# Performance work log

Hardware: AMD Instinct MI355X
Metric: run time of the kernel (lower is better)

The kernel has to match this reference:

```python
import jax, jax.numpy as jnp
import numpy as np

N, E, T, NORB, H, C = 10000, 100000, 200000, 9, 128, 64


def _normalize(v, eps=1e-12):
    # F.normalize: v / max(||v||_2, eps) along last dim
    n = jnp.linalg.norm(v, axis=-1, keepdims=True)
    return v / jnp.maximum(n, eps)


def setup_inputs() -> dict:
    key = jax.random.key(0)
    ks = jax.random.split(key, 24)
    p = lambda i, shape, scale=0.05: jax.random.normal(ks[i], shape, jnp.float32) * scale
    return {
        "x": jax.random.normal(ks[0], (N, H), jnp.float32),
        "cji": jax.random.normal(ks[1], (E, NORB, C), jnp.float32),
        "cutoff_w": jax.random.uniform(ks[2], (E,), jnp.float32),
        "rb": jax.random.normal(ks[3], (E, NORB), jnp.float32),
        "shb": jax.random.normal(ks[4], (T, NORB), jnp.float32),
        "idx_i": jax.random.randint(ks[5], (E,), 0, N),
        "idx_j": jax.random.randint(ks[6], (E,), 0, N),
        "tri_idx_k": jax.random.randint(ks[7], (T,), 0, N),
        "edge_idx_kj": jax.random.randint(ks[8], (T,), 0, E),
        "edge_idx_ji": jax.random.randint(ks[9], (T,), 0, E),
        "w_node": p(10, (H, 2 * C)),
        "b_node": jnp.zeros((2 * C,), jnp.float32),
        "w_c1": p(11, (C, C)),  # coeffs_dim == C here
        "w_c2": p(12, (C, C)),
        "w_t1": p(13, (C, C)),
        "b_t1": jnp.zeros((C,), jnp.float32),
        "w_t2": p(14, (C, C)),
        "b_t2": jnp.zeros((C,), jnp.float32),
        "w_basis": p(15, (C, C)),
        "w_n1": p(16, (2 * C, C)),
        "b_n1": jnp.zeros((C,), jnp.float32),
        "w_n2": p(17, (C, C)),
        "b_n2": jnp.zeros((C,), jnp.float32),
        "w_out": p(18, (C, H)),
    }


def reference(x, cji, cutoff_w, rb, shb, idx_i, idx_j, tri_idx_k, edge_idx_kj,
              edge_idx_ji, w_node, b_node, w_c1, w_c2, w_t1, b_t1, w_t2, b_t2,
              w_basis, w_n1, b_n1, w_n2, b_n2, w_out):
    silu = jax.nn.silu
    x_before = x
    # node_weight -> chunk into (x, xk), each (N, C)
    h = x @ w_node + b_node
    x1, xk = h[:, :C], h[:, C:]
    # f_coeffs: two bias-free Dense + SiLU, per (E, n_orb) position
    cji = silu(silu(cji @ w_c1) @ w_c2)  # (E, NORB, C)
    # cutoff weighting on radial basis
    rb = rb * cutoff_w[:, None]  # (E, NORB)
    # triplet gather + contraction over orbital axis d
    ckj = cji[edge_idx_kj]  # (T, NORB, C)
    three_body_orbs = jnp.einsum("td,tdh->th", rb[edge_idx_kj] * shb, ckj)  # (T, C)
    three_body_orbs = _normalize(three_body_orbs)
    xk_g = jax.nn.sigmoid(xk[tri_idx_k])  # (T, C)
    three_body_w = three_body_orbs * xk_g
    # scatter-sum triplets -> edges, then f_three MLP
    agg = jax.ops.segment_sum(three_body_w, edge_idx_ji, num_segments=E)  # (E, C)
    three_body_w = silu(silu(agg @ w_t1 + b_t1) @ w_t2 + b_t2)  # (E, C)
    cji = cji + cji * three_body_w[:, None, :]  # (E, NORB, C)
    # LCAO weights: contract radial basis with coefficients
    lcao_w = jnp.einsum("ed,edh->eh", rb, cji)  # (E, C)
    lcao_w = _normalize(lcao_w) @ w_basis
    # f_node on gathered endpoint features
    pair = jnp.concatenate([x1[idx_i], x1[idx_j]], axis=-1)  # (E, 2C)
    fnode = silu(silu(pair @ w_n1 + b_n1) @ w_n2 + b_n2)  # (E, C)
    msg = lcao_w * fnode
    out = x_before + jax.ops.segment_sum(msg, idx_i, num_segments=N) @ w_out
    return out
```

## Files before the change

### kernel.cpp

```cpp
#include <hip/hip_runtime.h>
#include <math.h>

typedef __attribute__((ext_vector_type(8))) short bf16x8;
typedef __attribute__((ext_vector_type(4))) float f32x4;
typedef __attribute__((ext_vector_type(4))) unsigned int uint32x4;
typedef unsigned int uint32;
typedef unsigned short ushort;

#define N_NODES 10000
#define E_EDGES 100000
#define T_TRI   200000
#define NORB    9
#define H_DIM   128
#define C_DIM   64
#define LSTR    68

__device__ __forceinline__ ushort f2b_rtne(float f) {
  uint32 u = __float_as_uint(f);
  u += 0x7FFFu + ((u >> 16) & 1u);
  return (ushort)(u >> 16);
}
__device__ __forceinline__ uint32 rtne2(float a, float b) {
  uint32 ua = __float_as_uint(a), ub = __float_as_uint(b);
  ua += 0x7FFFu + ((ua >> 16) & 1u);
  ub += 0x7FFFu + ((ub >> 16) & 1u);
  return (ua >> 16) | (ub & 0xFFFF0000u);
}
__device__ __forceinline__ uint32 trunc2(float a, float b) {
  return (__float_as_uint(a) >> 16) | (__float_as_uint(b) & 0xFFFF0000u);
}
__device__ __forceinline__ float b2f(ushort u) {
  return __uint_as_float(((uint32)u) << 16);
}
__device__ __forceinline__ float silu_f(float x) {
  return x * __builtin_amdgcn_rcpf(1.0f + __expf(-x));
}
__device__ __forceinline__ float sigmoid_f(float x) {
  return __builtin_amdgcn_rcpf(1.0f + __expf(-x));
}
__device__ __forceinline__ float rl(float v, int k) {
  return __uint_as_float(__builtin_amdgcn_readlane(__float_as_uint(v), k));
}
__device__ __forceinline__ f32x4 mfma16(bf16x8 a, bf16x8 b, f32x4 c) {
  return __builtin_amdgcn_mfma_f32_16x16x32_bf16(a, b, c, 0, 0, 0);
}
#define LDS_FENCE() asm volatile("s_waitcnt lgkmcnt(0)" ::: "memory")

__device__ __forceinline__ bf16x8 pack8(const float* p) {
  f32x4 v0 = *(const f32x4*)p;
  f32x4 v1 = *(const f32x4*)(p + 4);
  uint32x4 u;
  u[0] = trunc2(v0[0], v0[1]);
  u[1] = trunc2(v0[2], v0[3]);
  u[2] = trunc2(v1[0], v1[1]);
  u[3] = trunc2(v1[2], v1[3]);
  return __builtin_bit_cast(bf16x8, u);
}
__device__ __forceinline__ bf16x8 bfrag_w(const float* W, int kt, int ct, int lane) {
  const float* p = W + (size_t)(kt * 32 + ((lane >> 4) * 8)) * 64 + ct * 16 + (lane & 15);
  bf16x8 r;
#pragma unroll
  for (int b = 0; b < 8; ++b) r[b] = (short)f2b_rtne(p[(size_t)b * 64]);
  return r;
}

__global__ __launch_bounds__(128) void k_node_mlp(
    const float* __restrict__ x, const float* __restrict__ w_node,
    const float* __restrict__ b_node, ushort* __restrict__ x1b,
    ushort* __restrict__ sigxkb) {
  __shared__ float xs[H_DIM];
  int n = blockIdx.x;
  int c = threadIdx.x;
  xs[c] = x[(size_t)n * H_DIM + c];
  __syncthreads();
  float acc = b_node[c];
#pragma unroll 8
  for (int k = 0; k < H_DIM; ++k)
    acc = fmaf(xs[k], w_node[k * H_DIM + c], acc);
  if (c < C_DIM)
    x1b[(size_t)n * C_DIM + c] = f2b_rtne(acc);
  else
    sigxkb[(size_t)n * C_DIM + (c - C_DIM)] = f2b_rtne(sigmoid_f(acc));
}

__global__ __launch_bounds__(256) void k_cji_mlp_mfma(
    const float* __restrict__ cji, const float* __restrict__ w_c1,
    const float* __restrict__ w_c2, ushort* __restrict__ cji2) {
  __shared__ __align__(16) float lds_all[4][16 * LSTR];
  int lane = threadIdx.x & 63;
  float* lds = lds_all[threadIdx.x >> 6];
  int wid = (blockIdx.x * 256 + (int)threadIdx.x) >> 6;
  int nw = (gridDim.x * 256) >> 6;
  bf16x8 w1f[2][4], w2f[2][4];
#pragma unroll
  for (int kt = 0; kt < 2; ++kt)
#pragma unroll
    for (int ct = 0; ct < 4; ++ct) {
      w1f[kt][ct] = bfrag_w(w_c1, kt, ct, lane);
      w2f[kt][ct] = bfrag_w(w_c2, kt, ct, lane);
    }
  const int nstrips = (E_EDGES * NORB) / 16;
  int l15 = lane & 15, g = lane >> 4;
  int wrow = g * 4, wcol = l15;
  f32x4 z = {0.f, 0.f, 0.f, 0.f};
  for (int s = wid; s < nstrips; s += nw) {
    const float* ap = cji + (size_t)(s * 16 + l15) * 64 + g * 8;
    bf16x8 a0 = pack8(ap), a1 = pack8(ap + 32);
#pragma unroll
    for (int ct = 0; ct < 4; ++ct) {
      f32x4 acc = mfma16(a0, w1f[0][ct], z);
      acc = mfma16(a1, w1f[1][ct], acc);
#pragma unroll
      for (int r = 0; r < 4; ++r)
        lds[(wrow + r) * LSTR + ct * 16 + wcol] = silu_f(acc[r]);
    }
    LDS_FENCE();
    bf16x8 t0 = pack8(lds + l15 * LSTR + g * 8);
    bf16x8 t1 = pack8(lds + l15 * LSTR + 32 + g * 8);
#pragma unroll
    for (int ct = 0; ct < 4; ++ct) {
      f32x4 acc = mfma16(t0, w2f[0][ct], z);
      acc = mfma16(t1, w2f[1][ct], acc);
#pragma unroll
      for (int r = 0; r < 4; ++r)
        lds[(wrow + r) * LSTR + ct * 16 + wcol] = silu_f(acc[r]);
    }
    LDS_FENCE();
    const float* lp = lds + l15 * LSTR + g * 16;
    f32x4 v0 = *(const f32x4*)lp;
    f32x4 v1 = *(const f32x4*)(lp + 4);
    f32x4 v2 = *(const f32x4*)(lp + 8);
    f32x4 v3 = *(const f32x4*)(lp + 12);
    uint32x4 o0, o1;
    o0[0] = rtne2(v0[0], v0[1]); o0[1] = rtne2(v0[2], v0[3]);
    o0[2] = rtne2(v1[0], v1[1]); o0[3] = rtne2(v1[2], v1[3]);
    o1[0] = rtne2(v2[0], v2[1]); o1[1] = rtne2(v2[2], v2[3]);
    o1[2] = rtne2(v3[0], v3[1]); o1[3] = rtne2(v3[2], v3[3]);
    uint32x4* dst = (uint32x4*)(cji2 + (size_t)(s * 16 + l15) * 64 + g * 16);
    dst[0] = o0;
    dst[1] = o1;
  }
}

__global__ __launch_bounds__(256) void k_triplet(
    const ushort* __restrict__ cji2, const float* __restrict__ rb,
    const float* __restrict__ cutoff_w, const float* __restrict__ shb,
    const int* __restrict__ tri_idx_k, const int* __restrict__ edge_idx_kj,
    const int* __restrict__ edge_idx_ji, const ushort* __restrict__ sigxkb,
    float* __restrict__ agg) {
  int lane = threadIdx.x & 63;
  int wid = (blockIdx.x * 256 + (int)threadIdx.x) >> 6;
  int nw = (gridDim.x * 256) >> 6;
  for (int t = wid; t < T_TRI; t += nw) {
    int e = edge_idx_kj[t];
    float cw = cutoff_w[e];
    const ushort* crow = cji2 + (size_t)e * (NORB * C_DIM);
    float acc = 0.f;
#pragma unroll
    for (int d = 0; d < NORB; ++d) {
      float coeff = rb[e * NORB + d] * cw * shb[t * NORB + d];
      acc = fmaf(coeff, b2f(crow[d * C_DIM + lane]), acc);
    }
    float s = acc * acc;
#pragma unroll
    for (int m = 32; m >= 1; m >>= 1) s += __shfl_xor(s, m, 64);
    float scale = __builtin_amdgcn_rsqf(fmaxf(s, 1e-30f));
    int kn = tri_idx_k[t];
    float gxe = b2f(sigxkb[(size_t)kn * C_DIM + lane]);
    float val = acc * scale * gxe;
    int ej = edge_idx_ji[t];
    atomicAdd(&agg[(size_t)ej * C_DIM + lane], val);
  }
}

__global__ __launch_bounds__(256) void k_tbw_lcao(
    const float* __restrict__ agg, const float* __restrict__ w_t1,
    const float* __restrict__ b_t1, const float* __restrict__ w_t2,
    const float* __restrict__ b_t2, const ushort* __restrict__ cji2,
    const float* __restrict__ rb, const float* __restrict__ cutoff_w,
    const float* __restrict__ w_basis, float* __restrict__ lcao) {
  __shared__ __align__(16) float lds_all[4][16 * LSTR];
  int lane = threadIdx.x & 63;
  float* lds = lds_all[threadIdx.x >> 6];
  int wid = (blockIdx.x * 256 + (int)threadIdx.x) >> 6;
  int nw = (gridDim.x * 256) >> 6;
  bf16x8 wt1[2][4], wt2[2][4], wb[2][4];
  float bt1[4], bt2[4];
  int l15 = lane & 15, g = lane >> 4;
#pragma unroll
  for (int ct = 0; ct < 4; ++ct) {
    bt1[ct] = b_t1[ct * 16 + l15];
    bt2[ct] = b_t2[ct * 16 + l15];
#pragma unroll
    for (int kt = 0; kt < 2; ++kt) {
      wt1[kt][ct] = bfrag_w(w_t1, kt, ct, lane);
      wt2[kt][ct] = bfrag_w(w_t2, kt, ct, lane);
      wb[kt][ct] = bfrag_w(w_basis, kt, ct, lane);
    }
  }
  const int nstrips = E_EDGES / 16;
  int wrow = g * 4, wcol = l15;
  f32x4 z = {0.f, 0.f, 0.f, 0.f};
  for (int s = wid; s < nstrips; s += nw) {
    const float* ap = agg + (size_t)(s * 16 + l15) * 64 + g * 8;
    bf16x8 a0 = pack8(ap), a1 = pack8(ap + 32);
#pragma unroll
    for (int ct = 0; ct < 4; ++ct) {
      f32x4 acc = mfma16(a0, wt1[0][ct], z);
      acc = mfma16(a1, wt1[1][ct], acc);
#pragma unroll
      for (int r = 0; r < 4; ++r)
        lds[(wrow + r) * LSTR + ct * 16 + wcol] = silu_f(acc[r] + bt1[ct]);
    }
    LDS_FENCE();
    bf16x8 t0 = pack8(lds + l15 * LSTR + g * 8);
    bf16x8 t1 = pack8(lds + l15 * LSTR + 32 + g * 8);
    LDS_FENCE();
#pragma unroll
    for (int ct = 0; ct < 4; ++ct) {
      f32x4 acc = mfma16(t0, wt2[0][ct], z);
      acc = mfma16(t1, wt2[1][ct], acc);
#pragma unroll
      for (int r = 0; r < 4; ++r)
        lds[(wrow + r) * LSTR + ct * 16 + wcol] = silu_f(acc[r] + bt2[ct]);
    }
    LDS_FENCE();
    for (int ee = 0; ee < 16; ++ee) {
      int e = s * 16 + ee;
      float cw = cutoff_w[e];
      const ushort* crow = cji2 + (size_t)e * (NORB * C_DIM);
      float acc = 0.f;
#pragma unroll
      for (int d = 0; d < NORB; ++d)
        acc = fmaf(rb[e * NORB + d] * cw, b2f(crow[d * C_DIM + lane]), acc);
      acc *= (1.0f + lds[ee * LSTR + lane]);
      float ss = acc * acc;
#pragma unroll
      for (int m = 32; m >= 1; m >>= 1) ss += __shfl_xor(ss, m, 64);
      float scale = __builtin_amdgcn_rsqf(fmaxf(ss, 1e-30f));
      lds[ee * LSTR + lane] = acc * scale;
    }
    LDS_FENCE();
    bf16x8 n0 = pack8(lds + l15 * LSTR + g * 8);
    bf16x8 n1 = pack8(lds + l15 * LSTR + 32 + g * 8);
    LDS_FENCE();
    f32x4 o[4];
#pragma unroll
    for (int ct = 0; ct < 4; ++ct) {
      o[ct] = mfma16(n0, wb[0][ct], z);
      o[ct] = mfma16(n1, wb[1][ct], o[ct]);
#pragma unroll
      for (int r = 0; r < 4; ++r)
        lds[(wrow + r) * LSTR + ct * 16 + wcol] = o[ct][r];
    }
    LDS_FENCE();
    const float* lp = lds + l15 * LSTR + g * 16;
    f32x4* dst = (f32x4*)(lcao + (size_t)(s * 16 + l15) * 64 + g * 16);
    dst[0] = *(const f32x4*)lp;
    dst[1] = *(const f32x4*)(lp + 4);
    dst[2] = *(const f32x4*)(lp + 8);
    dst[3] = *(const f32x4*)(lp + 12);
  }
}

__global__ __launch_bounds__(256) void k_msg_mfma(
    const ushort* __restrict__ x1b, const int* __restrict__ idx_i,
    const int* __restrict__ idx_j, const float* __restrict__ w_n1,
    const float* __restrict__ b_n1, const float* __restrict__ w_n2,
    const float* __restrict__ b_n2, const float* __restrict__ lcao,
    float* __restrict__ nodeagg) {
  __shared__ __align__(16) float lds_all[4][16 * LSTR];
  int lane = threadIdx.x & 63;
  float* lds = lds_all[threadIdx.x >> 6];
  int wid = (blockIdx.x * 256 + (int)threadIdx.x) >> 6;
  int nw = (gridDim.x * 256) >> 6;
  bf16x8 wn1f[4][4], wn2f[2][4];
  float bn1[4], bn2[4];
  int l15 = lane & 15, g = lane >> 4;
#pragma unroll
  for (int ct = 0; ct < 4; ++ct) {
    bn1[ct] = b_n1[ct * 16 + l15];
    bn2[ct] = b_n2[ct * 16 + l15];
#pragma unroll
    for (int kt = 0; kt < 4; ++kt) wn1f[kt][ct] = bfrag_w(w_n1, kt, ct, lane);
#pragma unroll
    for (int kt = 0; kt < 2; ++kt) wn2f[kt][ct] = bfrag_w(w_n2, kt, ct, lane);
  }
  const int nstrips = E_EDGES / 16;
  int wrow = g * 4, wcol = l15;
  f32x4 z = {0.f, 0.f, 0.f, 0.f};
  for (int s = wid; s < nstrips; s += nw) {
    int er = s * 16 + l15;
    int ii = idx_i[er], jj = idx_j[er];
    const uint32x4* pi = (const uint32x4*)(x1b + (size_t)ii * 64 + g * 8);
    const uint32x4* pj = (const uint32x4*)(x1b + (size_t)jj * 64 + g * 8);
    bf16x8 a0 = __builtin_bit_cast(bf16x8, pi[0]);
    bf16x8 a1 = __builtin_bit_cast(bf16x8, pi[2]);
    bf16x8 a2 = __builtin_bit_cast(bf16x8, pj[0]);
    bf16x8 a3 = __builtin_bit_cast(bf16x8, pj[2]);
#pragma unroll
    for (int ct = 0; ct < 4; ++ct) {
      f32x4 acc = mfma16(a0, wn1f[0][ct], z);
      acc = mfma16(a1, wn1f[1][ct], acc);
      acc = mfma16(a2, wn1f[2][ct], acc);
      acc = mfma16(a3, wn1f[3][ct], acc);
#pragma unroll
      for (int r = 0; r < 4; ++r)
        lds[(wrow + r) * LSTR + ct * 16 + wcol] = silu_f(acc[r] + bn1[ct]);
    }
    LDS_FENCE();
    bf16x8 t0 = pack8(lds + l15 * LSTR + g * 8);
    bf16x8 t1 = pack8(lds + l15 * LSTR + 32 + g * 8);
    f32x4 acc2[4];
#pragma unroll
    for (int ct = 0; ct < 4; ++ct) {
      acc2[ct] = mfma16(t0, wn2f[0][ct], z);
      acc2[ct] = mfma16(t1, wn2f[1][ct], acc2[ct]);
    }
#pragma unroll
    for (int r = 0; r < 4; ++r) {
      int ge = s * 16 + wrow + r;
      int ni = idx_i[ge];
#pragma unroll
      for (int ct = 0; ct < 4; ++ct) {
        float f = silu_f(acc2[ct][r] + bn2[ct]);
        float m = lcao[(size_t)ge * 64 + ct * 16 + l15] * f;
        atomicAdd(&nodeagg[(size_t)ni * 64 + ct * 16 + l15], m);
      }
    }
  }
}

__global__ __launch_bounds__(256) void k_out(
    const float* __restrict__ x, const float* __restrict__ nodeagg,
    const float* __restrict__ w_out, float* __restrict__ out) {
  int lane = threadIdx.x & 63;
  int wid = (blockIdx.x * 256 + (int)threadIdx.x) >> 6;
  int nw = (gridDim.x * 256) >> 6;
  float wo0[64], wo1[64];
#pragma unroll
  for (int k = 0; k < 64; ++k) wo0[k] = w_out[k * H_DIM + lane];
#pragma unroll
  for (int k = 0; k < 64; ++k) wo1[k] = w_out[k * H_DIM + 64 + lane];
  for (int n = wid; n < N_NODES; n += nw) {
    float v = nodeagg[(size_t)n * 64 + lane];
    float a0 = 0.f, a1 = 0.f;
#pragma unroll
    for (int k = 0; k < 64; ++k) {
      float a = rl(v, k);
      a0 = fmaf(a, wo0[k], a0);
      a1 = fmaf(a, wo1[k], a1);
    }
    out[(size_t)n * H_DIM + lane] = x[(size_t)n * H_DIM + lane] + a0;
    out[(size_t)n * H_DIM + 64 + lane] = x[(size_t)n * H_DIM + 64 + lane] + a1;
  }
}

extern "C" void kernel_launch(void* const* d_in, const int* in_sizes, int n_in,
                              void* d_out, int out_size, void* d_ws, size_t ws_size,
                              hipStream_t stream) {
  const float* x         = (const float*)d_in[0];
  const float* cji       = (const float*)d_in[1];
  const float* cutoff_w  = (const float*)d_in[2];
  const float* rb        = (const float*)d_in[3];
  const float* shb       = (const float*)d_in[4];
  const int*   idx_i     = (const int*)d_in[5];
  const int*   idx_j     = (const int*)d_in[6];
  const int*   tri_idx_k = (const int*)d_in[7];
  const int*   e_kj      = (const int*)d_in[8];
  const int*   e_ji      = (const int*)d_in[9];
  const float* w_node    = (const float*)d_in[10];
  const float* b_node    = (const float*)d_in[11];
  const float* w_c1      = (const float*)d_in[12];
  const float* w_c2      = (const float*)d_in[13];
  const float* w_t1      = (const float*)d_in[14];
  const float* b_t1      = (const float*)d_in[15];
  const float* w_t2      = (const float*)d_in[16];
  const float* b_t2      = (const float*)d_in[17];
  const float* w_basis   = (const float*)d_in[18];
  const float* w_n1      = (const float*)d_in[19];
  const float* b_n1      = (const float*)d_in[20];
  const float* w_n2      = (const float*)d_in[21];
  const float* b_n2      = (const float*)d_in[22];
  const float* w_out     = (const float*)d_in[23];
  float* out = (float*)d_out;

  char* ws = (char*)d_ws;
  ushort* x1b    = (ushort*)(ws + 0);
  ushort* sigxkb = (ushort*)(ws + 1280000);
  ushort* cji2   = (ushort*)(ws + 2560000);
  float*  aggbuf = (float*)(ws + 117760000);
  float*  lcao   = (float*)(ws + 143360000);
  float*  nodeagg= (float*)(ws + 168960000);

  hipMemsetAsync(aggbuf, 0, (size_t)6400000 * sizeof(float), stream);
  hipMemsetAsync(nodeagg, 0, (size_t)640000 * sizeof(float), stream);

  k_node_mlp<<<N_NODES, 128, 0, stream>>>(x, w_node, b_node, x1b, sigxkb);
  k_cji_mlp_mfma<<<2048, 256, 0, stream>>>(cji, w_c1, w_c2, cji2);
  k_triplet<<<2048, 256, 0, stream>>>(cji2, rb, cutoff_w, shb, tri_idx_k, e_kj,
                                      e_ji, sigxkb, aggbuf);
  k_tbw_lcao<<<1024, 256, 0, stream>>>(aggbuf, w_t1, b_t1, w_t2, b_t2, cji2,
                                       rb, cutoff_w, w_basis, lcao);
  k_msg_mfma<<<1024, 256, 0, stream>>>(x1b, idx_i, idx_j, w_n1, b_n1, w_n2,
                                       b_n2, lcao, nodeagg);
  k_out<<<256, 256, 0, stream>>>(x, nodeagg, w_out, out);
}
```

Before: 296.6 us.

## Precompute rb-weighted cji sum in cji MLP, swap MFMA operands, bf16 LDS staging

Result: slower. 364.9 us (+23.0%).

```diff
diff --git a/kernel.cpp b/kernel.cpp
--- a/kernel.cpp
+++ b/kernel.cpp
@@ -3,7 +3,9 @@
 
 typedef __attribute__((ext_vector_type(8))) short bf16x8;
 typedef __attribute__((ext_vector_type(4))) float f32x4;
+typedef __attribute__((ext_vector_type(2))) float f32x2;
 typedef __attribute__((ext_vector_type(4))) unsigned int uint32x4;
+typedef __attribute__((ext_vector_type(2))) unsigned int uint32x2;
 typedef unsigned int uint32;
 typedef unsigned short ushort;
 
@@ -13,7 +15,7 @@
 #define NORB    9
 #define H_DIM   128
 #define C_DIM   64
-#define LSTR    68
+#define USTR    36
 
 __device__ __forceinline__ ushort f2b_rtne(float f) {
   uint32 u = __float_as_uint(f);
@@ -49,6 +51,14 @@
 __device__ __forceinline__ bf16x8 pack8(const float* p) {
   f32x4 v0 = *(const f32x4*)p;
   f32x4 v1 = *(const f32x4*)(p + 4);
+  uint32x4 u;
+  u[0] = trunc2(v0[0], v0[1]);
+  u[1] = trunc2(v0[2], v0[3]);
+  u[2] = trunc2(v1[0], v1[1]);
+  u[3] = trunc2(v1[2], v1[3]);
+  return __builtin_bit_cast(bf16x8, u);
+}
+__device__ __forceinline__ bf16x8 pack8v(f32x4 v0, f32x4 v1) {
   uint32x4 u;
   u[0] = trunc2(v0[0], v0[1]);
   u[1] = trunc2(v0[2], v0[3]);
@@ -83,12 +93,16 @@
     sigxkb[(size_t)n * C_DIM + (c - C_DIM)] = f2b_rtne(sigmoid_f(acc));
 }
 
-__global__ __launch_bounds__(256) void k_cji_mlp_mfma(
+__global__ __launch_bounds__(256) void k_cji_fused(
     const float* __restrict__ cji, const float* __restrict__ w_c1,
-    const float* __restrict__ w_c2, ushort* __restrict__ cji2) {
-  __shared__ __align__(16) float lds_all[4][16 * LSTR];
+    const float* __restrict__ w_c2, const float* __restrict__ rb,
+    const float* __restrict__ cutoff_w, ushort* __restrict__ cji2,
+    float* __restrict__ rbsum) {
+  __shared__ uint32 lds_all[4][2][16 * USTR];
   int lane = threadIdx.x & 63;
-  float* lds = lds_all[threadIdx.x >> 6];
+  int l15 = lane & 15, g = lane >> 4;
+  uint32* lds0 = lds_all[threadIdx.x >> 6][0];
+  uint32* lds1 = lds_all[threadIdx.x >> 6][1];
   int wid = (blockIdx.x * 256 + (int)threadIdx.x) >> 6;
   int nw = (gridDim.x * 256) >> 6;
   bf16x8 w1f[2][4], w2f[2][4];
@@ -99,46 +113,70 @@
       w1f[kt][ct] = bfrag_w(w_c1, kt, ct, lane);
       w2f[kt][ct] = bfrag_w(w_c2, kt, ct, lane);
     }
-  const int nstrips = (E_EDGES * NORB) / 16;
-  int l15 = lane & 15, g = lane >> 4;
-  int wrow = g * 4, wcol = l15;
+  uint32* cji2u = (uint32*)cji2;
+  const int nblk = E_EDGES / 16;
   f32x4 z = {0.f, 0.f, 0.f, 0.f};
-  for (int s = wid; s < nstrips; s += nw) {
-    const float* ap = cji + (size_t)(s * 16 + l15) * 64 + g * 8;
-    bf16x8 a0 = pack8(ap), a1 = pack8(ap + 32);
-#pragma unroll
-    for (int ct = 0; ct < 4; ++ct) {
-      f32x4 acc = mfma16(a0, w1f[0][ct], z);
-      acc = mfma16(a1, w1f[1][ct], acc);
-#pragma unroll
-      for (int r = 0; r < 4; ++r)
-        lds[(wrow + r) * LSTR + ct * 16 + wcol] = silu_f(acc[r]);
-    }
-    LDS_FENCE();
-    bf16x8 t0 = pack8(lds + l15 * LSTR + g * 8);
-    bf16x8 t1 = pack8(lds + l15 * LSTR + 32 + g * 8);
-#pragma unroll
-    for (int ct = 0; ct < 4; ++ct) {
-      f32x4 acc = mfma16(t0, w2f[0][ct], z);
-      acc = mfma16(t1, w2f[1][ct], acc);
-#pragma unroll
-      for (int r = 0; r < 4; ++r)
-        lds[(wrow + r) * LSTR + ct * 16 + wcol] = silu_f(acc[r]);
-    }
-    LDS_FENCE();
-    const float* lp = lds + l15 * LSTR + g * 16;
-    f32x4 v0 = *(const f32x4*)lp;
-    f32x4 v1 = *(const f32x4*)(lp + 4);
-    f32x4 v2 = *(const f32x4*)(lp + 8);
-    f32x4 v3 = *(const f32x4*)(lp + 12);
-    uint32x4 o0, o1;
-    o0[0] = rtne2(v0[0], v0[1]); o0[1] = rtne2(v0[2], v0[3]);
-    o0[2] = rtne2(v1[0], v1[1]); o0[3] = rtne2(v1[2], v1[3]);
-    o1[0] = rtne2(v2[0], v2[1]); o1[1] = rtne2(v2[2], v2[3]);
-    o1[2] = rtne2(v3[0], v3[1]); o1[3] = rtne2(v3[2], v3[3]);
-    uint32x4* dst = (uint32x4*)(cji2 + (size_t)(s * 16 + l15) * 64 + g * 16);
-    dst[0] = o0;
-    dst[1] = o1;
+  for (int eb = wid; eb < nblk; eb += nw) {
+    int e0 = eb * 16;
+    int myrow0 = 9 * (e0 + l15);
+    float cw = cutoff_w[e0 + l15];
+    f32x4 rs[4];
+#pragma unroll
+    for (int ct = 0; ct < 4; ++ct) rs[ct] = z;
+    const float* ap = cji + (size_t)myrow0 * 64 + g * 8;
+    f32x4 nv0 = *(const f32x4*)ap;
+    f32x4 nv1 = *(const f32x4*)(ap + 4);
+    f32x4 nv2 = *(const f32x4*)(ap + 32);
+    f32x4 nv3 = *(const f32x4*)(ap + 36);
+#pragma unroll
+    for (int d = 0; d < NORB; ++d) {
+      f32x4 c0 = nv0, c1 = nv1, c2 = nv2, c3 = nv3;
+      if (d < NORB - 1) {
+        const float* np = cji + (size_t)(myrow0 + d + 1) * 64 + g * 8;
+        nv0 = *(const f32x4*)np;
+        nv1 = *(const f32x4*)(np + 4);
+        nv2 = *(const f32x4*)(np + 32);
+        nv3 = *(const f32x4*)(np + 36);
+      }
+      bf16x8 a0 = pack8v(c0, c1), a1 = pack8v(c2, c3);
+      uint32* buf = (d & 1) ? lds1 : lds0;
+#pragma unroll
+      for (int ct = 0; ct < 4; ++ct) {
+        f32x4 acc = mfma16(w1f[0][ct], a0, z);
+        acc = mfma16(w1f[1][ct], a1, acc);
+        uint32x2 p;
+        p[0] = rtne2(silu_f(acc[0]), silu_f(acc[1]));
+        p[1] = rtne2(silu_f(acc[2]), silu_f(acc[3]));
+        *(uint32x2*)(buf + l15 * USTR + ct * 8 + 2 * g) = p;
+      }
+      LDS_FENCE();
+      bf16x8 t0 = *(const bf16x8*)(buf + l15 * USTR + 4 * g);
+      bf16x8 t1 = *(const bf16x8*)(buf + l15 * USTR + 16 + 4 * g);
+      float rbw = rb[(e0 + l15) * NORB + d] * cw;
+      int rowu = (myrow0 + d) * 32;
+#pragma unroll
+      for (int ct = 0; ct < 4; ++ct) {
+        f32x4 acc = mfma16(w2f[0][ct], t0, z);
+        acc = mfma16(w2f[1][ct], t1, acc);
+        float v0 = silu_f(acc[0]), v1 = silu_f(acc[1]);
+        float v2 = silu_f(acc[2]), v3 = silu_f(acc[3]);
+        uint32x2 p;
+        p[0] = rtne2(v0, v1);
+        p[1] = rtne2(v2, v3);
+        *(uint32x2*)(cji2u + rowu + ct * 8 + 2 * g) = p;
+        rs[ct][0] = fmaf(rbw, v0, rs[ct][0]);
+        rs[ct][1] = fmaf(rbw, v1, rs[ct][1]);
+        rs[ct][2] = fmaf(rbw, v2, rs[ct][2]);
+        rs[ct][3] = fmaf(rbw, v3, rs[ct][3]);
+      }
+    }
+    float* rp = rbsum + (size_t)(e0 + l15) * 64 + 4 * g;
+#pragma unroll
+    for (int ct = 0; ct < 4; ++ct) {
+      f32x2 q0 = {rs[ct][0], rs[ct][1]}, q1 = {rs[ct][2], rs[ct][3]};
+      *(f32x2*)(rp + ct * 16) = q0;
+      *(f32x2*)(rp + ct * 16 + 2) = q1;
+    }
   }
 }
 
@@ -176,21 +214,24 @@
 __global__ __launch_bounds__(256) void k_tbw_lcao(
     const float* __restrict__ agg, const float* __restrict__ w_t1,
     const float* __restrict__ b_t1, const float* __restrict__ w_t2,
-    const float* __restrict__ b_t2, const ushort* __restrict__ cji2,
-    const float* __restrict__ rb, const float* __restrict__ cutoff_w,
+    const float* __restrict__ b_t2, const float* __restrict__ rbsum,
     const float* __restrict__ w_basis, float* __restrict__ lcao) {
-  __shared__ __align__(16) float lds_all[4][16 * LSTR];
+  __shared__ uint32 lds_all[4][2][16 * USTR];
   int lane = threadIdx.x & 63;
-  float* lds = lds_all[threadIdx.x >> 6];
+  int l15 = lane & 15, g = lane >> 4;
+  uint32* lds0 = lds_all[threadIdx.x >> 6][0];
+  uint32* lds1 = lds_all[threadIdx.x >> 6][1];
   int wid = (blockIdx.x * 256 + (int)threadIdx.x) >> 6;
   int nw = (gridDim.x * 256) >> 6;
   bf16x8 wt1[2][4], wt2[2][4], wb[2][4];
-  float bt1[4], bt2[4];
-  int l15 = lane & 15, g = lane >> 4;
+  float bt1v[4][4], bt2v[4][4];
 #pragma unroll
   for (int ct = 0; ct < 4; ++ct) {
-    bt1[ct] = b_t1[ct * 16 + l15];
-    bt2[ct] = b_t2[ct * 16 + l15];
+#pragma unroll
+    for (int r = 0; r < 4; ++r) {
+      bt1v[ct][r] = b_t1[ct * 16 + 4 * g + r];
+      bt2v[ct][r] = b_t2[ct * 16 + 4 * g + r];
+    }
 #pragma unroll
     for (int kt = 0; kt < 2; ++kt) {
       wt1[kt][ct] = bfrag_w(w_t1, kt, ct, lane);
@@ -198,68 +239,62 @@
       wb[kt][ct] = bfrag_w(w_basis, kt, ct, lane);
     }
   }
-  const int nstrips = E_EDGES / 16;
-  int wrow = g * 4, wcol = l15;
+  const int nblk = E_EDGES / 16;
   f32x4 z = {0.f, 0.f, 0.f, 0.f};
-  for (int s = wid; s < nstrips; s += nw) {
-    const float* ap = agg + (size_t)(s * 16 + l15) * 64 + g * 8;
+  for (int eb = wid; eb < nblk; eb += nw) {
+    int e0 = eb * 16;
+    const float* ap = agg + (size_t)(e0 + l15) * 64 + g * 8;
     bf16x8 a0 = pack8(ap), a1 = pack8(ap + 32);
 #pragma unroll
     for (int ct = 0; ct < 4; ++ct) {
-      f32x4 acc = mfma16(a0, wt1[0][ct], z);
-      acc = mfma16(a1, wt1[1][ct], acc);
-#pragma unroll
-      for (int r = 0; r < 4; ++r)
-        lds[(wrow + r) * LSTR + ct * 16 + wcol] = silu_f(acc[r] + bt1[ct]);
+      f32x4 acc = mfma16(wt1[0][ct], a0, z);
+      acc = mfma16(wt1[1][ct], a1, acc);
+      uint32x2 p;
+      p[0] = rtne2(silu_f(acc[0] + bt1v[ct][0]), silu_f(acc[1] + bt1v[ct][1]));
+      p[1] = rtne2(silu_f(acc[2] + bt1v[ct][2]), silu_f(acc[3] + bt1v[ct][3]));
+      *(uint32x2*)(lds0 + l15 * USTR + ct * 8 + 2 * g) = p;
     }
     LDS_FENCE();
-    bf16x8 t0 = pack8(lds + l15 * LSTR + g * 8);
-    bf16x8 t1 = pack8(lds + l15 * LSTR + 32 + g * 8);
+    bf16x8 t0 = *(const bf16x8*)(lds0 + l15 * USTR + 4 * g);
+    bf16x8 t1 = *(const bf16x8*)(lds0 + l15 * USTR + 16 + 4 * g);
+    const float* rp = rbsum + (size_t)(e0 + l15) * 64 + 4 * g;
+    f32x4 val[4];
+    float ss = 0.f;
+#pragma unroll
+    for (int ct = 0; ct < 4; ++ct) {
+      f32x4 acc = mfma16(wt2[0][ct], t0, z);
+      acc = mfma16(wt2[1][ct], t1, acc);
+      f32x2 q0 = *(const f32x2*)(rp + ct * 16);
+      f32x2 q1 = *(const f32x2*)(rp + ct * 16 + 2);
+      val[ct][0] = q0[0] * (1.0f + silu_f(acc[0] + bt2v[ct][0]));
+      val[ct][1] = q0[1] * (1.0f + silu_f(acc[1] + bt2v[ct][1]));
+      val[ct][2] = q1[0] * (1.0f + silu_f(acc[2] + bt2v[ct][2]));
+      val[ct][3] = q1[1] * (1.0f + silu_f(acc[3] + bt2v[ct][3]));
+      ss += val[ct][0] * val[ct][0] + val[ct][1] * val[ct][1] +
+            val[ct][2] * val[ct][2] + val[ct][3] * val[ct][3];
+    }
+    ss += __shfl_xor(ss, 16, 64);
+    ss += __shfl_xor(ss, 32, 64);
+    float scale = __builtin_amdgcn_rsqf(fmaxf(ss, 1e-30f));
+#pragma unroll
+    for (int ct = 0; ct < 4; ++ct) {
+      uint32x2 p;
+      p[0] = rtne2(val[ct][0] * scale, val[ct][1] * scale);
+      p[1] = rtne2(val[ct][2] * scale, val[ct][3] * scale);
+      *(uint32x2*)(lds1 + l15 * USTR + ct * 8 + 2 * g) = p;
+    }
     LDS_FENCE();
-#pragma unroll
-    for (int ct = 0; ct < 4; ++ct) {
-      f32x4 acc = mfma16(t0, wt2[0][ct], z);
-      acc = mfma16(t1, wt2[1][ct], acc);
-#pragma unroll
-      for (int r = 0; r < 4; ++r)
-        lds[(wrow + r) * LSTR + ct * 16 + wcol] = silu_f(acc[r] + bt2[ct]);
-    }
-    LDS_FENCE();
-    for (int ee = 0; ee < 16; ++ee) {
-      int e = s * 16 + ee;
-      float cw = cutoff_w[e];
-      const ushort* crow = cji2 + (size_t)e * (NORB * C_DIM);
-      float acc = 0.f;
-#pragma unroll
-      for (int d = 0; d < NORB; ++d)
-        acc = fmaf(rb[e * NORB + d] * cw, b2f(crow[d * C_DIM + lane]), acc);
-      acc *= (1.0f + lds[ee * LSTR + lane]);
-      float ss = acc * acc;
-#pragma unroll
-      for (int m = 32; m >= 1; m >>= 1) ss += __shfl_xor(ss, m, 64);
-      float scale = __builtin_amdgcn_rsqf(fmaxf(ss, 1e-30f));
-      lds[ee * LSTR + lane] = acc * scale;
-    }
-    LDS_FENCE();
-    bf16x8 n0 = pack8(lds + l15 * LSTR + g * 8);
-    bf16x8 n1 = pack8(lds + l15 * LSTR + 32 + g * 8);
-    LDS_FENCE();
-    f32x4 o[4];
-#pragma unroll
-    for (int ct = 0; ct < 4; ++ct) {
-      o[ct] = mfma16(n0, wb[0][ct], z);
-      o[ct] = mfma16(n1, wb[1][ct], o[ct]);
-#pragma unroll
-      for (int r = 0; r < 4; ++r)
-        lds[(wrow + r) * LSTR + ct * 16 + wcol] = o[ct][r];
-    }
-    LDS_FENCE();
-    const float* lp = lds + l15 * LSTR + g * 16;
-    f32x4* dst = (f32x4*)(lcao + (size_t)(s * 16 + l15) * 64 + g * 16);
-    dst[0] = *(const f32x4*)lp;
-    dst[1] = *(const f32x4*)(lp + 4);
-    dst[2] = *(const f32x4*)(lp + 8);
-    dst[3] = *(const f32x4*)(lp + 12);
+    bf16x8 n0 = *(const bf16x8*)(lds1 + l15 * USTR + 4 * g);
+    bf16x8 n1 = *(const bf16x8*)(lds1 + l15 * USTR + 16 + 4 * g);
+    float* lp = lcao + (size_t)(e0 + l15) * 64 + 4 * g;
+#pragma unroll
+    for (int ct = 0; ct < 4; ++ct) {
+      f32x4 o = mfma16(wb[0][ct], n0, z);
+      o = mfma16(wb[1][ct], n1, o);
+      f32x2 q0 = {o[0], o[1]}, q1 = {o[2], o[3]};
+      *(f32x2*)(lp + ct * 16) = q0;
+      *(f32x2*)(lp + ct * 16 + 2) = q1;
+    }
   }
 }
 
@@ -269,28 +304,36 @@
     const float* __restrict__ b_n1, const float* __restrict__ w_n2,
     const float* __restrict__ b_n2, const float* __restrict__ lcao,
     float* __restrict__ nodeagg) {
-  __shared__ __align__(16) float lds_all[4][16 * LSTR];
+  __shared__ uint32 lds_all[4][16 * USTR];
   int lane = threadIdx.x & 63;
-  float* lds = lds_all[threadIdx.x >> 6];
+  int l15 = lane & 15, g = lane >> 4;
+  uint32* lds = lds_all[threadIdx.x >> 6];
   int wid = (blockIdx.x * 256 + (int)threadIdx.x) >> 6;
   int nw = (gridDim.x * 256) >> 6;
   bf16x8 wn1f[4][4], wn2f[2][4];
-  float bn1[4], bn2[4];
-  int l15 = lane & 15, g = lane >> 4;
+  float bn1v[4][4], bn2v[4][4];
 #pragma unroll
   for (int ct = 0; ct < 4; ++ct) {
-    bn1[ct] = b_n1[ct * 16 + l15];
-    bn2[ct] = b_n2[ct * 16 + l15];
-#pragma unroll
-    for (int kt = 0; kt < 4; ++kt) wn1f[kt][ct] = bfrag_w(w_n1, kt, ct, lane);
+#pragma unroll
+    for (int r = 0; r < 4; ++r) {
+      bn1v[ct][r] = b_n1[ct * 16 + 4 * g + r];
+      bn2v[ct][r] = b_n2[ct * 16 + 4 * g + r];
+    }
+#pragma unroll
+    for (int kt = 0; kt < 4; ++kt) {
+      const float* p = w_n1 + (size_t)(kt * 32 + g * 8) * 64 + ct * 16 + l15;
+      bf16x8 r8;
+#pragma unroll
+      for (int b = 0; b < 8; ++b) r8[b] = (short)f2b_rtne(p[(size_t)b * 64]);
+      wn1f[kt][ct] = r8;
+    }
 #pragma unroll
     for (int kt = 0; kt < 2; ++kt) wn2f[kt][ct] = bfrag_w(w_n2, kt, ct, lane);
   }
-  const int nstrips = E_EDGES / 16;
-  int wrow = g * 4, wcol = l15;
+  const int nblk = E_EDGES / 16;
   f32x4 z = {0.f, 0.f, 0.f, 0.f};
-  for (int s = wid; s < nstrips; s += nw) {
-    int er = s * 16 + l15;
+  for (int eb = wid; eb < nblk; eb += nw) {
+    int er = eb * 16 + l15;
     int ii = idx_i[er], jj = idx_j[er];
     const uint32x4* pi = (const uint32x4*)(x1b + (size_t)ii * 64 + g * 8);
     const uint32x4* pj = (const uint32x4*)(x1b + (size_t)jj * 64 + g * 8);
@@ -300,33 +343,31 @@
     bf16x8 a3 = __builtin_bit_cast(bf16x8, pj[2]);
 #pragma unroll
     for (int ct = 0; ct < 4; ++ct) {
-      f32x4 acc = mfma16(a0, wn1f[0][ct], z);
-      acc = mfma16(a1, wn1f[1][ct], acc);
-      acc = mfma16(a2, wn1f[2][ct], acc);
-      acc = mfma16(a3, wn1f[3][ct], acc);
-#pragma unroll
-      for (int r = 0; r < 4; ++r)
-        lds[(wrow + r) * LSTR + ct * 16 + wcol] = silu_f(acc[r] + bn1[ct]);
+      f32x4 acc = mfma16(wn1f[0][ct], a0, z);
+      acc = mfma16(wn1f[1][ct], a1, acc);
+      acc = mfma16(wn1f[2][ct], a2, acc);
+      acc = mfma16(wn1f[3][ct], a3, acc);
+      uint32x2 p;
+      p[0] = rtne2(silu_f(acc[0] + bn1v[ct][0]), silu_f(acc[1] + bn1v[ct][1]));
+      p[1] = rtne2(silu_f(acc[2] + bn1v[ct][2]), silu_f(acc[3] + bn1v[ct][3]));
+      *(uint32x2*)(lds + l15 * USTR + ct * 8 + 2 * g) = p;
     }
     LDS_FENCE();
-    bf16x8 t0 = pack8(lds + l15 * LSTR + g * 8);
-    bf16x8 t1 = pack8(lds + l15 * LSTR + 32 + g * 8);
-    f32x4 acc2[4];
-#pragma unroll
-    for (int ct = 0; ct < 4; ++ct) {
-      acc2[ct] = mfma16(t0, wn2f[0][ct], z);
-      acc2[ct] = mfma16(t1, wn2f[1][ct], acc2[ct]);
-    }
-#pragma unroll
-    for (int r = 0; r < 4; ++r) {
-      int ge = s * 16 + wrow + r;
-      int ni = idx_i[ge];
-#pragma unroll
-      for (int ct = 0; ct < 4; ++ct) {
-        float f = silu_f(acc2[ct][r] + bn2[ct]);
-        float m = lcao[(size_t)ge * 64 + ct * 16 + l15] * f;
-        atomicAdd(&nodeagg[(size_t)ni * 64 + ct * 16 + l15], m);
-      }
+    bf16x8 t0 = *(const bf16x8*)(lds + l15 * USTR + 4 * g);
+    bf16x8 t1 = *(const bf16x8*)(lds + l15 * USTR + 16 + 4 * g);
+    LDS_FENCE();
+    const float* lp = lcao + (size_t)er * 64 + 4 * g;
+    float* np = nodeagg + (size_t)ii * 64 + 4 * g;
+#pragma unroll
+    for (int ct = 0; ct < 4; ++ct) {
+      f32x4 acc = mfma16(wn2f[0][ct], t0, z);
+      acc = mfma16(wn2f[1][ct], t1, acc);
+      f32x2 q0 = *(const f32x2*)(lp + ct * 16);
+      f32x2 q1 = *(const f32x2*)(lp + ct * 16 + 2);
+      atomicAdd(np + ct * 16 + 0, q0[0] * silu_f(acc[0] + bn2v[ct][0]));
+      atomicAdd(np + ct * 16 + 1, q0[1] * silu_f(acc[1] + bn2v[ct][1]));
+      atomicAdd(np + ct * 16 + 2, q1[0] * silu_f(acc[2] + bn2v[ct][2]));
+      atomicAdd(np + ct * 16 + 3, q1[1] * silu_f(acc[3] + bn2v[ct][3]));
     }
   }
 }
@@ -390,18 +431,20 @@
   ushort* sigxkb = (ushort*)(ws + 1280000);
   ushort* cji2   = (ushort*)(ws + 2560000);
   float*  aggbuf = (float*)(ws + 117760000);
-  float*  lcao   = (float*)(ws + 143360000);
-  float*  nodeagg= (float*)(ws + 168960000);
+  float*  rbsum  = (float*)(ws + 143360000);
+  float*  lcao   = (float*)(ws + 168960000);
+  float*  nodeagg= (float*)(ws + 194560000);
 
   hipMemsetAsync(aggbuf, 0, (size_t)6400000 * sizeof(float), stream);
   hipMemsetAsync(nodeagg, 0, (size_t)640000 * sizeof(float), stream);
 
   k_node_mlp<<<N_NODES, 128, 0, stream>>>(x, w_node, b_node, x1b, sigxkb);
-  k_cji_mlp_mfma<<<2048, 256, 0, stream>>>(cji, w_c1, w_c2, cji2);
+  k_cji_fused<<<1568, 256, 0, stream>>>(cji, w_c1, w_c2, rb, cutoff_w, cji2,
+                                        rbsum);
   k_triplet<<<2048, 256, 0, stream>>>(cji2, rb, cutoff_w, shb, tri_idx_k, e_kj,
                                       e_ji, sigxkb, aggbuf);
-  k_tbw_lcao<<<1024, 256, 0, stream>>>(aggbuf, w_t1, b_t1, w_t2, b_t2, cji2,
-                                       rb, cutoff_w, w_basis, lcao);
+  k_tbw_lcao<<<392, 256, 0, stream>>>(aggbuf, w_t1, b_t1, w_t2, b_t2, rbsum,
+                                      w_basis, lcao);
   k_msg_mfma<<<1024, 256, 0, stream>>>(x1b, idx_i, idx_j, w_n1, b_n1, w_n2,
                                        b_n2, lcao, nodeagg);
   k_out<<<256, 256, 0, stream>>>(x, nodeagg, w_out, out);
```
